# Kernel tuning notes

Measured on AMD Instinct MI355X. Metric: run time of the kernel, lower is better.

## Reference

```python
import jax, jax.numpy as jnp
import numpy as np

NUM_HEADS = 12
EPS = 1e-4


def setup_inputs() -> dict:
    key = jax.random.key(0)
    k1, k2, k3 = jax.random.split(key, 3)
    C = 768
    B, N = 128, 196  # B = b * num_frames = 8 * 16
    x = jax.random.normal(k1, (B, N, C), dtype=jnp.float32)
    W_qkv = jax.random.normal(k2, (3 * C, C), dtype=jnp.float32) * 0.02
    W_proj = jax.random.normal(k3, (C, C), dtype=jnp.float32) * 0.02
    b_proj = jnp.zeros((C,), dtype=jnp.float32)
    return {"x": x, "W_qkv": W_qkv, "W_proj": W_proj, "b_proj": b_proj,
            "num_frames": 16}


def reference(x, W_qkv, W_proj, b_proj, num_frames):
    B, N, C = x.shape
    h = NUM_HEADS
    e = C // h
    # qkv projection (no bias), split k-first then heads: 'b n (k h e)'
    qkv = (x @ W_qkv.T).reshape(B, N, 3, h, e)
    q, k, v = qkv[:, :, 0], qkv[:, :, 1], qkv[:, :, 2]  # [B, N, h, e]
    q_ = jax.nn.relu(q)
    k_ = jax.nn.relu(k)
    # fold frames into the sequence: (b f) n -> b (f n)
    b = B // num_frames
    S = num_frames * N
    q_ = q_.reshape(b, S, h, e)
    k_ = k_.reshape(b, S, h, e)
    v_ = v.reshape(b, S, h, e)
    # kv trick: kv[b,h,e,d] = sum_s k[b,s,h,e] v[b,s,h,d]
    kv = jnp.einsum('bshe,bshd->bhed', k_, v_)
    k_sum = k_.sum(axis=1)  # [b, h, e]
    z = 1.0 / (jnp.einsum('bshe,bhe->bsh', q_, k_sum) + EPS)  # [b, S, h]
    out = jnp.einsum('bshe,bhed->bshd', q_, kv) * z[..., None]  # [b, S, h, e]
    out = out.reshape(B, N, C)
    # output projection (dropouts are identity at eval)
    return out @ W_proj.T + b_proj
```

## Files before the change

### kernel.cpp

```cpp
#include <hip/hip_runtime.h>
#include <hip/hip_bf16.h>

#define EPS_Z 1e-4f

typedef __attribute__((ext_vector_type(8))) short bf16x8;
typedef __attribute__((ext_vector_type(4))) float f32x4;

__device__ __forceinline__ float b2f(short s) {
    union { unsigned u; float f; } cv;
    cv.u = ((unsigned)(unsigned short)s) << 16;
    return cv.f;
}

__device__ __forceinline__ void gld_lds16(const __hip_bfloat16* g, __hip_bfloat16* l) {
    __builtin_amdgcn_global_load_lds(
        (__attribute__((address_space(1))) void*)(g),
        (__attribute__((address_space(3))) void*)(l),
        16, 0, 0);
}

__global__ __launch_bounds__(256)
void cvt_f32_bf16(const float* __restrict__ in, __hip_bfloat16* __restrict__ out, int n4)
{
    int i = blockIdx.x * 256 + threadIdx.x;
    if (i >= n4) return;
    float4 v = ((const float4*)in)[i];
    union { short4 s; __hip_bfloat16 h[4]; } o;
    o.h[0] = __float2bfloat16(v.x);
    o.h[1] = __float2bfloat16(v.y);
    o.h[2] = __float2bfloat16(v.z);
    o.h[3] = __float2bfloat16(v.w);
    ((short4*)out)[i] = o.s;
}

template<int MODE, typename CT>
__global__ __launch_bounds__(256, 2)
void gemm_bt(const __hip_bfloat16* __restrict__ A,
             const __hip_bfloat16* __restrict__ B,
             CT* __restrict__ C,
             const float* __restrict__ bias,
             int K, int N)
{
    __shared__ __align__(16) __hip_bfloat16 As[128 * 64];
    __shared__ __align__(16) __hip_bfloat16 Bs[128 * 64];
    const int tid = threadIdx.x;
    const int w = tid >> 6;
    const int l = tid & 63;
    const int wr = (w >> 1) * 64;
    const int wc = (w & 1) * 64;
    const int l15 = l & 15;
    const int lq = l >> 4;
    const int rx = l15 & 7;

    f32x4 acc[4][4] = {};

    const int srow8 = l >> 3;
    const int scol = (((l & 7) ^ (l >> 3)) << 3);

    const __hip_bfloat16* Ab = A + (size_t)blockIdx.y * 128 * K;
    const __hip_bfloat16* Bb = B + (size_t)blockIdx.x * 128 * K;

    for (int k0 = 0; k0 < K; k0 += 64) {
        __syncthreads();
        #pragma unroll
        for (int i = 0; i < 4; ++i) {
            const int chunk = w * 4 + i;
            const int row = chunk * 8 + srow8;
            gld_lds16(Ab + (size_t)row * K + (k0 + scol), As + chunk * 512);
            gld_lds16(Bb + (size_t)row * K + (k0 + scol), Bs + chunk * 512);
        }
        __syncthreads();
        #pragma unroll
        for (int kk = 0; kk < 64; kk += 32) {
            const int kb = (kk >> 3) + lq;
            const int col = (kb ^ rx) << 3;
            bf16x8 a[4], b[4];
            #pragma unroll
            for (int i = 0; i < 4; ++i)
                a[i] = *(const bf16x8*)(As + (wr + i * 16 + l15) * 64 + col);
            #pragma unroll
            for (int j = 0; j < 4; ++j)
                b[j] = *(const bf16x8*)(Bs + (wc + j * 16 + l15) * 64 + col);
            #pragma unroll
            for (int i = 0; i < 4; ++i)
                #pragma unroll
                for (int j = 0; j < 4; ++j)
                    acc[i][j] = __builtin_amdgcn_mfma_f32_16x16x32_bf16(a[i], b[j], acc[i][j], 0, 0, 0);
        }
    }

    const int crow0 = blockIdx.y * 128 + wr + lq * 4;
    const int ccol0 = blockIdx.x * 128 + wc + l15;
    #pragma unroll
    for (int i = 0; i < 4; ++i) {
        #pragma unroll
        for (int j = 0; j < 4; ++j) {
            const int gc = ccol0 + j * 16;
            const float badd = (MODE == 2) ? bias[gc] : 0.0f;
            #pragma unroll
            for (int r = 0; r < 4; ++r) {
                const int gr = crow0 + i * 16 + r;
                float v = acc[i][j][r];
                if (MODE == 1 && gc < 1536) v = fmaxf(v, 0.0f);
                if (MODE == 2) v += badd;
                if (MODE == 1)
                    ((__hip_bfloat16*)C)[(size_t)gr * N + gc] = __float2bfloat16(v);
                else
                    ((float*)C)[(size_t)gr * N + gc] = v;
            }
        }
    }
}

__global__ __launch_bounds__(256, 2)
void kv_mfma_kernel(const __hip_bfloat16* __restrict__ qkv,
                    float* __restrict__ kvg, float* __restrict__ ksumg)
{
    const int SPLIT = 7;
    const int bh = blockIdx.x / SPLIT;
    const int ck = blockIdx.x % SPLIT;
    const int b = bh / 12, h = bh % 12;

    __shared__ __align__(16) __hip_bfloat16 kT[64 * 40];
    __shared__ __align__(16) __hip_bfloat16 vT[64 * 40];

    const int tid = threadIdx.x;
    const int w = tid >> 6, l = tid & 63;
    const int l15 = l & 15, lq = l >> 4;

    const int half = tid >> 7;
    const int idx  = tid & 127;
    const int e0 = (idx >> 4) * 8;
    const int sp = idx & 15;

    const size_t rowbase = (size_t)b * 3136 * 2304 + (half ? 1536 : 768) + h * 64 + e0;
    __hip_bfloat16* Tdst = half ? vT : kT;

    f32x4 acc[4] = {};
    f32x4 accks = {};

    bf16x8 ones;
    #pragma unroll
    for (int i = 0; i < 8; ++i) ones[i] = (short)0x3F80;

    const int s_begin = ck * 448;
    for (int s0 = s_begin; s0 < s_begin + 448; s0 += 32) {
        __syncthreads();
        bf16x8 r0 = *(const bf16x8*)(qkv + rowbase + (size_t)(s0 + 2 * sp) * 2304);
        bf16x8 r1 = *(const bf16x8*)(qkv + rowbase + (size_t)(s0 + 2 * sp + 1) * 2304);
        #pragma unroll
        for (int q = 0; q < 8; ++q) {
            unsigned pk = ((unsigned)(unsigned short)r0[q]) |
                          (((unsigned)(unsigned short)r1[q]) << 16);
            *(unsigned*)(Tdst + (e0 + q) * 40 + 2 * sp) = pk;
        }
        __syncthreads();
        bf16x8 a = *(const bf16x8*)(vT + (w * 16 + l15) * 40 + lq * 8);
        bf16x8 bfr[4];
        #pragma unroll
        for (int j = 0; j < 4; ++j)
            bfr[j] = *(const bf16x8*)(kT + (j * 16 + l15) * 40 + lq * 8);
        #pragma unroll
        for (int j = 0; j < 4; ++j)
            acc[j] = __builtin_amdgcn_mfma_f32_16x16x32_bf16(a, bfr[j], acc[j], 0, 0, 0);
        accks = __builtin_amdgcn_mfma_f32_16x16x32_bf16(ones, bfr[w], accks, 0, 0, 0);
    }

    float* kvdst = kvg + ((size_t)bh << 12);
    #pragma unroll
    for (int j = 0; j < 4; ++j) {
        const int col = j * 16 + l15;
        #pragma unroll
        for (int r = 0; r < 4; ++r) {
            const int row = w * 16 + lq * 4 + r;
            atomicAdd(kvdst + row * 64 + col, acc[j][r]);
        }
    }
    if (lq == 0)
        atomicAdd(ksumg + (bh << 6) + w * 16 + l15, accks[0]);
}

__global__ __launch_bounds__(256, 2)
void attn_mfma_kernel(const __hip_bfloat16* __restrict__ qkv,
                      const float* __restrict__ kvg,
                      const float* __restrict__ ksumg,
                      __hip_bfloat16* __restrict__ att)
{
    const int bh = blockIdx.x / 49;
    const int mt = blockIdx.x % 49;
    const int b = bh / 12, h = bh % 12;

    __shared__ __align__(16) __hip_bfloat16 qs[64 * 72];
    __shared__ __align__(16) __hip_bfloat16 kvs[64 * 72];
    __shared__ float kss[64];
    __shared__ float zrec[64];

    const int tid = threadIdx.x;
    const int w = tid >> 6, l = tid & 63;
    const int l15 = l & 15, lq = l >> 4;

    const size_t m0 = (size_t)b * 3136 + (size_t)mt * 64;

    {
        const int r = tid >> 2, c0 = (tid & 3) * 16;
        const __hip_bfloat16* src = qkv + (m0 + r) * 2304 + h * 64 + c0;
        bf16x8 t0 = *(const bf16x8*)(src);
        bf16x8 t1 = *(const bf16x8*)(src + 8);
        *(bf16x8*)(qs + r * 72 + c0) = t0;
        *(bf16x8*)(qs + r * 72 + c0 + 8) = t1;

        const float* kvsrc = kvg + ((size_t)bh << 12) + r * 64 + c0;
        float4 f0 = *(const float4*)(kvsrc);
        float4 f1 = *(const float4*)(kvsrc + 4);
        float4 f2 = *(const float4*)(kvsrc + 8);
        float4 f3 = *(const float4*)(kvsrc + 12);
        union { bf16x8 v; __hip_bfloat16 h[8]; } p0, p1;
        p0.h[0] = __float2bfloat16(f0.x); p0.h[1] = __float2bfloat16(f0.y);
        p0.h[2] = __float2bfloat16(f0.z); p0.h[3] = __float2bfloat16(f0.w);
        p0.h[4] = __float2bfloat16(f1.x); p0.h[5] = __float2bfloat16(f1.y);
        p0.h[6] = __float2bfloat16(f1.z); p0.h[7] = __float2bfloat16(f1.w);
        p1.h[0] = __float2bfloat16(f2.x); p1.h[1] = __float2bfloat16(f2.y);
        p1.h[2] = __float2bfloat16(f2.z); p1.h[3] = __float2bfloat16(f2.w);
        p1.h[4] = __float2bfloat16(f3.x); p1.h[5] = __float2bfloat16(f3.y);
        p1.h[6] = __float2bfloat16(f3.z); p1.h[7] = __float2bfloat16(f3.w);
        *(bf16x8*)(kvs + r * 72 + c0) = p0.v;
        *(bf16x8*)(kvs + r * 72 + c0 + 8) = p1.v;

        if (tid < 64) kss[tid] = ksumg[(bh << 6) + tid];
    }
    __syncthreads();

    if (tid < 64) {
        float zd = EPS_Z;
        #pragma unroll
        for (int c = 0; c < 8; ++c) {
            bf16x8 qv = *(const bf16x8*)(qs + tid * 72 + c * 8);
            #pragma unroll
            for (int j2 = 0; j2 < 8; ++j2) zd += b2f(qv[j2]) * kss[c * 8 + j2];
        }
        zrec[tid] = 1.0f / zd;
    }

    f32x4 acc[4] = {};
    #pragma unroll
    for (int ks = 0; ks < 2; ++ks) {
        bf16x8 a = *(const bf16x8*)(qs + (w * 16 + l15) * 72 + ks * 32 + lq * 8);
        #pragma unroll
        for (int j = 0; j < 4; ++j) {
            bf16x8 bb = *(const bf16x8*)(kvs + (j * 16 + l15) * 72 + ks * 32 + lq * 8);
            acc[j] = __builtin_amdgcn_mfma_f32_16x16x32_bf16(a, bb, acc[j], 0, 0, 0);
        }
    }
    __syncthreads();

    #pragma unroll
    for (int j = 0; j < 4; ++j) {
        const int col = j * 16 + l15;
        #pragma unroll
        for (int r = 0; r < 4; ++r) {
            const int row = w * 16 + lq * 4 + r;
            const float v = acc[j][r] * zrec[row];
            att[(m0 + row) * 768 + h * 64 + col] = __float2bfloat16(v);
        }
    }
}

extern "C" void kernel_launch(void* const* d_in, const int* in_sizes, int n_in,
                              void* d_out, int out_size, void* d_ws, size_t ws_size,
                              hipStream_t stream)
{
    const float* x      = (const float*)d_in[0];
    const float* W_qkv  = (const float*)d_in[1];
    const float* W_proj = (const float*)d_in[2];
    const float* b_proj = (const float*)d_in[3];
    float* out = (float*)d_out;

    const int M = 25088, K = 768, N1 = 2304, N2 = 768;

    __hip_bfloat16* qkv = (__hip_bfloat16*)d_ws;
    __hip_bfloat16* xb  = qkv + (size_t)M * N1;
    __hip_bfloat16* wqb = xb + (size_t)M * K;
    __hip_bfloat16* wpb = wqb + (size_t)N1 * K;
    float* kvg  = (float*)(wpb + (size_t)N2 * K);
    float* ksum = kvg + 96 * 4096;
    __hip_bfloat16* att = xb;

    hipMemsetAsync(kvg, 0, (size_t)(96 * 4096 + 96 * 64) * sizeof(float), stream);

    cvt_f32_bf16<<<(M * K / 4 + 255) / 256, 256, 0, stream>>>(x, xb, M * K / 4);
    cvt_f32_bf16<<<(N1 * K / 4 + 255) / 256, 256, 0, stream>>>(W_qkv, wqb, N1 * K / 4);
    cvt_f32_bf16<<<(N2 * K / 4 + 255) / 256, 256, 0, stream>>>(W_proj, wpb, N2 * K / 4);

    gemm_bt<1, __hip_bfloat16><<<dim3(N1 / 128, M / 128), 256, 0, stream>>>(xb, wqb, qkv, nullptr, K, N1);
    kv_mfma_kernel<<<96 * 7, 256, 0, stream>>>(qkv, kvg, ksum);
    attn_mfma_kernel<<<96 * 49, 256, 0, stream>>>(qkv, kvg, ksum, att);
    gemm_bt<2, float><<<dim3(N2 / 128, M / 128), 256, 0, stream>>>(att, wpb, out, b_proj, K, N2);
}
```

Measured before the change: 358.3 us.

## Remap GEMM blocks across XCDs, split kv finer, and simplify attention kernel

The GEMM launches switch to a 1D grid whose block index is permuted so consecutive tiles land on the same XCD (g&7 interleave), improving L2 reuse of A/B tiles. The kv reduction kernel doubles its sequence split to 14 chunks for more parallelism, at the cost of more atomics. A separate conversion kernel turns kv into bf16 once, and the attention kernel now loads q and kv fragments straight from global memory into registers with no LDS staging or barriers, computing the normalizer with wave shuffles. This adds one extra small kernel launch.

```diff
diff --git a/kernel.cpp b/kernel.cpp
--- a/kernel.cpp
+++ b/kernel.cpp
@@ -39,10 +39,15 @@
              const __hip_bfloat16* __restrict__ B,
              CT* __restrict__ C,
              const float* __restrict__ bias,
-             int K, int N)
+             int K, int N, int gx)
 {
     __shared__ __align__(16) __hip_bfloat16 As[128 * 64];
     __shared__ __align__(16) __hip_bfloat16 Bs[128 * 64];
+    const int g = blockIdx.x;
+    const int gp = (g & 7) * ((int)gridDim.x >> 3) + (g >> 3);
+    const int bx = gp % gx;
+    const int by = gp / gx;
+
     const int tid = threadIdx.x;
     const int w = tid >> 6;
     const int l = tid & 63;
@@ -57,8 +62,8 @@
     const int srow8 = l >> 3;
     const int scol = (((l & 7) ^ (l >> 3)) << 3);
 
-    const __hip_bfloat16* Ab = A + (size_t)blockIdx.y * 128 * K;
-    const __hip_bfloat16* Bb = B + (size_t)blockIdx.x * 128 * K;
+    const __hip_bfloat16* Ab = A + (size_t)by * 128 * K;
+    const __hip_bfloat16* Bb = B + (size_t)bx * 128 * K;
 
     for (int k0 = 0; k0 < K; k0 += 64) {
         __syncthreads();
@@ -89,8 +94,8 @@
         }
     }
 
-    const int crow0 = blockIdx.y * 128 + wr + lq * 4;
-    const int ccol0 = blockIdx.x * 128 + wc + l15;
+    const int crow0 = by * 128 + wr + lq * 4;
+    const int ccol0 = bx * 128 + wc + l15;
     #pragma unroll
     for (int i = 0; i < 4; ++i) {
         #pragma unroll
@@ -112,11 +117,11 @@
     }
 }
 
-__global__ __launch_bounds__(256, 2)
+__global__ __launch_bounds__(256)
 void kv_mfma_kernel(const __hip_bfloat16* __restrict__ qkv,
                     float* __restrict__ kvg, float* __restrict__ ksumg)
 {
-    const int SPLIT = 7;
+    const int SPLIT = 14;
     const int bh = blockIdx.x / SPLIT;
     const int ck = blockIdx.x % SPLIT;
     const int b = bh / 12, h = bh % 12;
@@ -143,8 +148,8 @@
     #pragma unroll
     for (int i = 0; i < 8; ++i) ones[i] = (short)0x3F80;
 
-    const int s_begin = ck * 448;
-    for (int s0 = s_begin; s0 < s_begin + 448; s0 += 32) {
+    const int s_begin = ck * 224;
+    for (int s0 = s_begin; s0 < s_begin + 224; s0 += 32) {
         __syncthreads();
         bf16x8 r0 = *(const bf16x8*)(qkv + rowbase + (size_t)(s0 + 2 * sp) * 2304);
         bf16x8 r1 = *(const bf16x8*)(qkv + rowbase + (size_t)(s0 + 2 * sp + 1) * 2304);
@@ -180,87 +185,60 @@
         atomicAdd(ksumg + (bh << 6) + w * 16 + l15, accks[0]);
 }
 
-__global__ __launch_bounds__(256, 2)
-void attn_mfma_kernel(const __hip_bfloat16* __restrict__ qkv,
-                      const float* __restrict__ kvg,
-                      const float* __restrict__ ksumg,
-                      __hip_bfloat16* __restrict__ att)
+__global__ __launch_bounds__(256)
+void attn_mfma2(const __hip_bfloat16* __restrict__ qkv,
+                const __hip_bfloat16* __restrict__ kvb,
+                const float* __restrict__ ksumg,
+                __hip_bfloat16* __restrict__ att)
 {
     const int bh = blockIdx.x / 49;
     const int mt = blockIdx.x % 49;
     const int b = bh / 12, h = bh % 12;
-
-    __shared__ __align__(16) __hip_bfloat16 qs[64 * 72];
-    __shared__ __align__(16) __hip_bfloat16 kvs[64 * 72];
-    __shared__ float kss[64];
-    __shared__ float zrec[64];
-
     const int tid = threadIdx.x;
     const int w = tid >> 6, l = tid & 63;
     const int l15 = l & 15, lq = l >> 4;
 
-    const size_t m0 = (size_t)b * 3136 + (size_t)mt * 64;
-
-    {
-        const int r = tid >> 2, c0 = (tid & 3) * 16;
-        const __hip_bfloat16* src = qkv + (m0 + r) * 2304 + h * 64 + c0;
-        bf16x8 t0 = *(const bf16x8*)(src);
-        bf16x8 t1 = *(const bf16x8*)(src + 8);
-        *(bf16x8*)(qs + r * 72 + c0) = t0;
-        *(bf16x8*)(qs + r * 72 + c0 + 8) = t1;
-
-        const float* kvsrc = kvg + ((size_t)bh << 12) + r * 64 + c0;
-        float4 f0 = *(const float4*)(kvsrc);
-        float4 f1 = *(const float4*)(kvsrc + 4);
-        float4 f2 = *(const float4*)(kvsrc + 8);
-        float4 f3 = *(const float4*)(kvsrc + 12);
-        union { bf16x8 v; __hip_bfloat16 h[8]; } p0, p1;
-        p0.h[0] = __float2bfloat16(f0.x); p0.h[1] = __float2bfloat16(f0.y);
-        p0.h[2] = __float2bfloat16(f0.z); p0.h[3] = __float2bfloat16(f0.w);
-        p0.h[4] = __float2bfloat16(f1.x); p0.h[5] = __float2bfloat16(f1.y);
-        p0.h[6] = __float2bfloat16(f1.z); p0.h[7] = __float2bfloat16(f1.w);
-        p1.h[0] = __float2bfloat16(f2.x); p1.h[1] = __float2bfloat16(f2.y);
-        p1.h[2] = __float2bfloat16(f2.z); p1.h[3] = __float2bfloat16(f2.w);
-        p1.h[4] = __float2bfloat16(f3.x); p1.h[5] = __float2bfloat16(f3.y);
-        p1.h[6] = __float2bfloat16(f3.z); p1.h[7] = __float2bfloat16(f3.w);
-        *(bf16x8*)(kvs + r * 72 + c0) = p0.v;
-        *(bf16x8*)(kvs + r * 72 + c0 + 8) = p1.v;
-
-        if (tid < 64) kss[tid] = ksumg[(bh << 6) + tid];
-    }
-    __syncthreads();
-
-    if (tid < 64) {
-        float zd = EPS_Z;
-        #pragma unroll
-        for (int c = 0; c < 8; ++c) {
-            bf16x8 qv = *(const bf16x8*)(qs + tid * 72 + c * 8);
-            #pragma unroll
-            for (int j2 = 0; j2 < 8; ++j2) zd += b2f(qv[j2]) * kss[c * 8 + j2];
-        }
-        zrec[tid] = 1.0f / zd;
-    }
-
+    const size_t m0 = (size_t)b * 3136 + (size_t)mt * 64 + w * 16;
+
+    const __hip_bfloat16* qrow = qkv + (m0 + l15) * 2304 + h * 64;
+    bf16x8 aq0 = *(const bf16x8*)(qrow + lq * 8);
+    bf16x8 aq1 = *(const bf16x8*)(qrow + 32 + lq * 8);
+
+    const float* ks = ksumg + (bh << 6);
+    float kse[8], kse1[8];
+    *(float4*)(kse)      = *(const float4*)(ks + lq * 8);
+    *(float4*)(kse + 4)  = *(const float4*)(ks + lq * 8 + 4);
+    *(float4*)(kse1)     = *(const float4*)(ks + 32 + lq * 8);
+    *(float4*)(kse1 + 4) = *(const float4*)(ks + 32 + lq * 8 + 4);
+    float zp = 0.0f;
+    #pragma unroll
+    for (int j = 0; j < 8; ++j)
+        zp += b2f(aq0[j]) * kse[j] + b2f(aq1[j]) * kse1[j];
+    zp += __shfl_xor(zp, 16);
+    zp += __shfl_xor(zp, 32);
+    const float zr = 1.0f / (zp + EPS_Z);
+
+    const __hip_bfloat16* kvh = kvb + ((size_t)bh << 12);
     f32x4 acc[4] = {};
     #pragma unroll
-    for (int ks = 0; ks < 2; ++ks) {
-        bf16x8 a = *(const bf16x8*)(qs + (w * 16 + l15) * 72 + ks * 32 + lq * 8);
-        #pragma unroll
-        for (int j = 0; j < 4; ++j) {
-            bf16x8 bb = *(const bf16x8*)(kvs + (j * 16 + l15) * 72 + ks * 32 + lq * 8);
-            acc[j] = __builtin_amdgcn_mfma_f32_16x16x32_bf16(a, bb, acc[j], 0, 0, 0);
-        }
-    }
-    __syncthreads();
+    for (int j = 0; j < 4; ++j) {
+        bf16x8 b0 = *(const bf16x8*)(kvh + (j * 16 + l15) * 64 + lq * 8);
+        bf16x8 b1 = *(const bf16x8*)(kvh + (j * 16 + l15) * 64 + 32 + lq * 8);
+        acc[j] = __builtin_amdgcn_mfma_f32_16x16x32_bf16(aq0, b0, acc[j], 0, 0, 0);
+        acc[j] = __builtin_amdgcn_mfma_f32_16x16x32_bf16(aq1, b1, acc[j], 0, 0, 0);
+    }
+
+    float zrow[4];
+    #pragma unroll
+    for (int r = 0; r < 4; ++r) zrow[r] = __shfl(zr, lq * 4 + r);
 
     #pragma unroll
     for (int j = 0; j < 4; ++j) {
         const int col = j * 16 + l15;
         #pragma unroll
         for (int r = 0; r < 4; ++r) {
-            const int row = w * 16 + lq * 4 + r;
-            const float v = acc[j][r] * zrec[row];
-            att[(m0 + row) * 768 + h * 64 + col] = __float2bfloat16(v);
+            const int row = lq * 4 + r;
+            att[(m0 + row) * 768 + h * 64 + col] = __float2bfloat16(acc[j][r] * zrow[r]);
         }
     }
 }
@@ -283,6 +261,7 @@
     __hip_bfloat16* wpb = wqb + (size_t)N1 * K;
     float* kvg  = (float*)(wpb + (size_t)N2 * K);
     float* ksum = kvg + 96 * 4096;
+    __hip_bfloat16* kvb = (__hip_bfloat16*)(ksum + 96 * 64);
     __hip_bfloat16* att = xb;
 
     hipMemsetAsync(kvg, 0, (size_t)(96 * 4096 + 96 * 64) * sizeof(float), stream);
@@ -291,8 +270,11 @@
     cvt_f32_bf16<<<(N1 * K / 4 + 255) / 256, 256, 0, stream>>>(W_qkv, wqb, N1 * K / 4);
     cvt_f32_bf16<<<(N2 * K / 4 + 255) / 256, 256, 0, stream>>>(W_proj, wpb, N2 * K / 4);
 
-    gemm_bt<1, __hip_bfloat16><<<dim3(N1 / 128, M / 128), 256, 0, stream>>>(xb, wqb, qkv, nullptr, K, N1);
-    kv_mfma_kernel<<<96 * 7, 256, 0, stream>>>(qkv, kvg, ksum);
-    attn_mfma_kernel<<<96 * 49, 256, 0, stream>>>(qkv, kvg, ksum, att);
-    gemm_bt<2, float><<<dim3(N2 / 128, M / 128), 256, 0, stream>>>(att, wpb, out, b_proj, K, N2);
-}
+    gemm_bt<1, __hip_bfloat16><<<(M / 128) * (N1 / 128), 256, 0, stream>>>(
+        xb, wqb, qkv, nullptr, K, N1, N1 / 128);
+    kv_mfma_kernel<<<96 * 14, 256, 0, stream>>>(qkv, kvg, ksum);
+    cvt_f32_bf16<<<(96 * 4096 / 4 + 255) / 256, 256, 0, stream>>>(kvg, kvb, 96 * 4096 / 4);
+    attn_mfma2<<<96 * 49, 256, 0, stream>>>(qkv, kvb, ksum, att);
+    gemm_bt<2, float><<<(M / 128) * (N2 / 128), 256, 0, stream>>>(
+        att, wpb, out, b_proj, K, N2, N2 / 128);
+}
```

Measured after the change: 345.6 us. 3.5% less time.
